# Kernel optimization log

Measured on AMD Instinct MI355X. Metric: run time of the kernel, lower is better.

Reference implementation:

```python
import jax, jax.numpy as jnp
import numpy as np

EPS = 1e-6


def setup_inputs() -> dict:
    key = jax.random.key(0)
    ks = jax.random.split(key, 10)
    N1, N2, K, E, LAYERS = 4096, 4096, 10, 262144, 3
    D = 2 ** K  # 1024
    us = jax.random.uniform(ks[0], (LAYERS, N1, D), dtype=jnp.float32)
    vs = jax.random.uniform(ks[1], (LAYERS, N2, D), dtype=jnp.float32)
    gamma = jax.random.normal(ks[2], (N1, LAYERS), dtype=jnp.float32)
    delta = jax.random.normal(ks[3], (N2, LAYERS), dtype=jnp.float32)
    latent_z1 = jax.random.uniform(ks[4], (N1, LAYERS), dtype=jnp.float32)
    latent_w1 = jax.random.uniform(ks[5], (N2, LAYERS), dtype=jnp.float32)
    # p_k_l initialized as log(uniform) in torch; any real values are valid params
    p_ks = jnp.full((LAYERS, K + 1), jnp.log(1.0 / (K + 1)), dtype=jnp.float32)
    p_ks = p_ks + 0.01 * jax.random.normal(ks[6], (LAYERS, K + 1), dtype=jnp.float32)
    L_ = 5.0 * jnp.ones((1,), dtype=jnp.float32)
    sparse_is = jax.random.randint(ks[7], (LAYERS, E), 0, N1, dtype=jnp.int64) if jax.config.jax_enable_x64 else jax.random.randint(ks[7], (LAYERS, E), 0, N1).astype(jnp.int32)
    sparse_js = jax.random.randint(ks[8], (LAYERS, E), 0, N2).astype(sparse_is.dtype)
    return {"us": us, "vs": vs, "gamma": gamma, "delta": delta,
            "latent_z1": latent_z1, "latent_w1": latent_w1,
            "p_ks": p_ks, "L_": L_,
            "sparse_is": sparse_is, "sparse_js": sparse_js}


def reference(us, vs, gamma, delta, latent_z1, latent_w1, p_ks, L_, sparse_is, sparse_js):
    LAYERS, N1, D = us.shape
    N2 = vs.shape[1]
    K = p_ks.shape[1] - 1  # tree_height
    latent_z = jax.nn.softmax(latent_z1, axis=1)  # Softmax(dim=1)
    latent_w = jax.nn.softmax(latent_w1, axis=1)
    L = jax.nn.softplus(L_)[0]
    ll = jnp.float32(0.0)
    for layer in range(LAYERS):
        p_k = jax.nn.softmax(p_ks[layer], axis=0)  # soft_0
        g = gamma[:, layer]                         # [N1]
        d = delta[:, layer]                         # [N2]
        emb_z = jax.nn.softmax(us[layer], axis=1)   # [N1, D]
        emb_w = jax.nn.softmax(vs[layer], axis=1)   # [N2, D]
        # hierarchical tree-weighted similarity: sum of GEMMs at coarsening levels
        inter = p_k[0] * jnp.ones((N1, N2), dtype=us.dtype)
        z_k, w_k = emb_z, emb_w
        for k in range(1, K):
            z_k = z_k.reshape(N1, -1, 2).sum(axis=2)  # [N1, D/2^k]
            w_k = w_k.reshape(N2, -1, 2).sum(axis=2)  # [N2, D/2^k]
            inter = inter + p_k[k] * jnp.einsum('nd,md->nm', z_k, w_k + EPS)
        inter = inter + p_k[K] * jnp.einsum('nd,md->nm', emb_z, emb_w + EPS)
        mat_1 = g[:, None] + d[None, :]                              # [N1, N2]
        mat_0 = (latent_z[:, layer][:, None] * L) * (latent_w[:, layer] + EPS)[None, :] * inter
        mat = jax.nn.softplus(mat_0 + mat_1)
        z_pdist1 = mat.sum()
        if N1 == N2:  # remove diagonal contributions
            z_pdist1 = z_pdist1 - jnp.trace(mat)
        i_ = sparse_is[layer]
        j_ = sparse_js[layer]
        z_pdist2 = (mat_0[i_, j_] + mat_1[i_, j_]).sum()
        ll = ll + (z_pdist2 - z_pdist1)
    return ll
```

## Files before the change

### kernel.cpp

```cpp
#include <hip/hip_runtime.h>
#include <hip/hip_bf16.h>
#include <stdint.h>

#define EPSV 1e-6f
#define N1 4096
#define N2 4096
#define DD 1024
#define NLAYERS 3
#define KKC 10

typedef __bf16 bf16_t;
typedef __bf16 bf16x8 __attribute__((ext_vector_type(8)));
typedef float f32x4 __attribute__((ext_vector_type(4)));
typedef long longx2 __attribute__((ext_vector_type(2)));

#define ZSCALE 256.0f
#define WSCALE 64.0f
#define INVSCALE 6.103515625e-05f

#define NBIN_L 1024
#define NBIN_T (NLAYERS*NBIN_L)

__device__ __forceinline__ float softplus_fast(float x) {
  return fmaxf(x, 0.f) + __logf(1.f + __expf(-fabsf(x)));
}
__device__ __forceinline__ float softplus_ref(float x) {
  return fmaxf(x, 0.f) + log1pf(expf(-fabsf(x)));
}
__device__ __forceinline__ float wredsum(float x) {
  #pragma unroll
  for (int o = 32; o; o >>= 1) x += __shfl_xor(x, o, 64);
  return x;
}
__device__ __forceinline__ float wredmax(float x) {
  #pragma unroll
  for (int o = 32; o; o >>= 1) x = fmaxf(x, __shfl_xor(x, o, 64));
  return x;
}
__device__ __forceinline__ void global_load_lds16(const void* g, void* l) {
  __builtin_amdgcn_global_load_lds(
      (const __attribute__((address_space(1))) uint32_t*)g,
      (__attribute__((address_space(3))) uint32_t*)l, 16, 0, 0);
}

__device__ __forceinline__ uint32_t enc_e4m3(float x) {
  if (x < 0.015625f) return (uint32_t)__float2int_rn(x * 512.0f);
  uint32_t u = __float_as_uint(x);
  u += 0x7FFFFu + ((u >> 20) & 1u);
  return (((u >> 23) - 120u) << 3) | ((u >> 20) & 7u);
}

__global__ __launch_bounds__(256) void prep_small(
    const float* __restrict__ lz, const float* __restrict__ lw,
    const float* __restrict__ gamma, const float* __restrict__ delta,
    const float* __restrict__ pks, const float* __restrict__ Lp,
    float* __restrict__ consts, float* __restrict__ a_tab, float* __restrict__ b_tab,
    float* __restrict__ g_tab, float* __restrict__ d_tab,
    uint32_t* __restrict__ hist, float* __restrict__ out)
{
  int n = blockIdx.x * blockDim.x + threadIdx.x;
  float Lv = softplus_ref(Lp[0]);
  if (n == 0) out[0] = 0.f;
  if (n < NBIN_T) hist[n] = 0u;
  if (n < N1) {
    float z0 = lz[n*3], z1 = lz[n*3+1], z2 = lz[n*3+2];
    float m = fmaxf(z0, fmaxf(z1, z2));
    float e0 = expf(z0-m), e1 = expf(z1-m), e2 = expf(z2-m);
    float inv = 1.f/(e0+e1+e2);
    a_tab[0*N1+n] = e0*inv*Lv; a_tab[1*N1+n] = e1*inv*Lv; a_tab[2*N1+n] = e2*inv*Lv;
    float w0 = lw[n*3], w1 = lw[n*3+1], w2 = lw[n*3+2];
    m = fmaxf(w0, fmaxf(w1, w2));
    e0 = expf(w0-m); e1 = expf(w1-m); e2 = expf(w2-m);
    inv = 1.f/(e0+e1+e2);
    b_tab[0*N2+n] = e0*inv+EPSV; b_tab[1*N2+n] = e1*inv+EPSV; b_tab[2*N2+n] = e2*inv+EPSV;
    #pragma unroll
    for (int k = 0; k < 3; ++k) {
      g_tab[k*N1+n] = gamma[n*3+k];
      d_tab[k*N2+n] = delta[n*3+k];
    }
  }
  if (n < NLAYERS) {
    float p[KKC+1]; float m = -1e30f;
    for (int k = 0; k <= KKC; ++k) { p[k] = pks[n*(KKC+1)+k]; m = fmaxf(m, p[k]); }
    float s = 0.f;
    for (int k = 0; k <= KKC; ++k) { p[k] = expf(p[k]-m); s += p[k]; }
    float inv = 1.f/s;
    for (int k = 0; k <= KKC; ++k) consts[8 + n*(KKC+1) + k] = p[k]*inv;
    consts[n] = p[0]*inv + EPSV*(1.f - p[0]*inv);
  }
}

#define EPB 2048

__global__ __launch_bounds__(256) void edge_hist(
    const int* __restrict__ is_, const int* __restrict__ js_,
    uint32_t* __restrict__ hist, int E)
{
  __shared__ uint32_t h[NBIN_L];
  const int lay = blockIdx.y;
  const int t = threadIdx.x;
  #pragma unroll
  for (int i = 0; i < NBIN_L/256; ++i) h[t + i*256] = 0u;
  __syncthreads();
  const int e0 = blockIdx.x * EPB;
  const int e1 = min(e0 + EPB, E);
  for (int e = e0 + t; e < e1; e += 256) {
    int i = is_[(size_t)lay*E + e], j = js_[(size_t)lay*E + e];
    atomicAdd(&h[(i>>7)*32 + (j>>7)], 1u);
  }
  __syncthreads();
  #pragma unroll
  for (int i = 0; i < NBIN_L/256; ++i)
    if (h[t + i*256]) atomicAdd(&hist[lay*NBIN_L + t + i*256], h[t + i*256]);
}

__global__ __launch_bounds__(256) void edge_scan(
    const uint32_t* __restrict__ hist, uint32_t* __restrict__ off,
    uint32_t* __restrict__ cursor)
{
  __shared__ uint32_t sa[NBIN_T], sb[NBIN_T];
  const int t = threadIdx.x;
  for (int i = t; i < NBIN_T; i += 256) sa[i] = hist[i];
  __syncthreads();
  uint32_t* src = sa; uint32_t* dst = sb;
  for (int s = 1; s < NBIN_T; s <<= 1) {
    for (int i = t; i < NBIN_T; i += 256) dst[i] = src[i] + (i >= s ? src[i-s] : 0u);
    __syncthreads();
    uint32_t* tmp = src; src = dst; dst = tmp;
  }
  for (int i = t; i < NBIN_T; i += 256) {
    uint32_t ex = i ? src[i-1] : 0u;
    off[i] = ex; cursor[i] = ex;
  }
  if (t == 0) off[NBIN_T] = src[NBIN_T-1];
}

__global__ __launch_bounds__(256) void edge_scatter(
    const int* __restrict__ is_, const int* __restrict__ js_,
    uint32_t* __restrict__ cursor, uint16_t* __restrict__ ebuf, int E)
{
  __shared__ uint32_t h[NBIN_L];
  __shared__ uint32_t basev[NBIN_L];
  const int lay = blockIdx.y;
  const int t = threadIdx.x;
  #pragma unroll
  for (int i = 0; i < NBIN_L/256; ++i) h[t + i*256] = 0u;
  __syncthreads();
  const int e0 = blockIdx.x * EPB;
  const int e1 = min(e0 + EPB, E);
  for (int e = e0 + t; e < e1; e += 256) {
    int i = is_[(size_t)lay*E + e], j = js_[(size_t)lay*E + e];
    atomicAdd(&h[(i>>7)*32 + (j>>7)], 1u);
  }
  __syncthreads();
  #pragma unroll
  for (int i = 0; i < NBIN_L/256; ++i) {
    int b = t + i*256;
    basev[b] = h[b] ? atomicAdd(&cursor[lay*NBIN_L + b], h[b]) : 0u;
    h[b] = 0u;
  }
  __syncthreads();
  for (int e = e0 + t; e < e1; e += 256) {
    int i = is_[(size_t)lay*E + e], j = js_[(size_t)lay*E + e];
    int b = (i>>7)*32 + (j>>7);
    uint32_t r = atomicAdd(&h[b], 1u);
    ebuf[basev[b] + r] = (uint16_t)(((i & 127) << 7) | (j & 127));
  }
}

__global__ __launch_bounds__(256) void prep_rows(
    const float* __restrict__ us, const float* __restrict__ vs,
    uint8_t* __restrict__ zt8, uint8_t* __restrict__ wt8, size_t lstride,
    const float* __restrict__ consts, int layer0)
{
  const int t = threadIdx.x, w = t >> 6, l = t & 63;
  const int n = blockIdx.x*4 + w;
  const int layer = layer0 + blockIdx.y;
  const int zmode = (blockIdx.z == 0);
  const float* src = (zmode ? us : vs) + ((size_t)layer*N1 + n)*DD + l*16;
  uint8_t* drow = (zmode ? zt8 : wt8) + (size_t)blockIdx.y*lstride + (size_t)n*1024;
  const int p0 = (l>>2)*64 + ((l&1)*2)*16 + ((l&3)>>1)*8;

  float e[16];
  {
    const float4* s4 = (const float4*)src;
    float4 u0 = s4[0], u1 = s4[1], u2 = s4[2], u3 = s4[3];
    e[0]=u0.x; e[1]=u0.y; e[2]=u0.z; e[3]=u0.w;
    e[4]=u1.x; e[5]=u1.y; e[6]=u1.z; e[7]=u1.w;
    e[8]=u2.x; e[9]=u2.y; e[10]=u2.z; e[11]=u2.w;
    e[12]=u3.x; e[13]=u3.y; e[14]=u3.z; e[15]=u3.w;
  }
  float mx = e[0];
  #pragma unroll
  for (int i = 1; i < 16; ++i) mx = fmaxf(mx, e[i]);
  mx = wredmax(mx);
  float s = 0.f;
  #pragma unroll
  for (int i = 0; i < 16; ++i) { e[i] = __expf(e[i]-mx); s += e[i]; }
  s = wredsum(s);
  float inv = 1.f/s;
  #pragma unroll
  for (int i = 0; i < 16; ++i) e[i] *= inv;

  uint32_t b4[4] = {0u, 0u, 0u, 0u};
  if (!zmode) {
    #pragma unroll
    for (int i = 0; i < 16; ++i)
      b4[i>>2] |= enc_e4m3(e[i]*WSCALE) << ((i&3)*8);
  } else {
    float s1[8], s2[4], s3[2], s4v;
    #pragma unroll
    for (int i = 0; i < 8; ++i) s1[i] = e[2*i] + e[2*i+1];
    #pragma unroll
    for (int i = 0; i < 4; ++i) s2[i] = s1[2*i] + s1[2*i+1];
    s3[0] = s2[0]+s2[1]; s3[1] = s2[2]+s2[3];
    s4v = s3[0]+s3[1];
    float s5 = s4v + __shfl_xor(s4v, 1, 64);
    float s6 = s5  + __shfl_xor(s5, 2, 64);
    float s7 = s6  + __shfl_xor(s6, 4, 64);
    float s8 = s7  + __shfl_xor(s7, 8, 64);
    float s9 = s8  + __shfl_xor(s8, 16, 64);
    const float* pk = consts + 8 + layer*(KKC+1);
    const float base = pk[4]*s4v + pk[5]*s5 + pk[6]*s6 + pk[7]*s7 + pk[8]*s8 + pk[9]*s9;
    const float p1 = pk[1], p2 = pk[2], p3 = pk[3], p10 = pk[10];
    #pragma unroll
    for (int i = 0; i < 16; ++i) {
      float v = p10*e[i] + p1*s1[i>>1] + p2*s2[i>>2] + p3*s3[i>>3] + base;
      b4[i>>2] |= enc_e4m3(v*ZSCALE) << ((i&3)*8);
    }
  }
  uint64_t u0 = (uint64_t)b4[0] | ((uint64_t)b4[1] << 32);
  uint64_t u1 = (uint64_t)b4[2] | ((uint64_t)b4[3] << 32);
  *(uint64_t*)(drow + p0)      = u0;
  *(uint64_t*)(drow + p0 + 16) = u1;
}

__global__ __launch_bounds__(256, 4) void gemm_fused(
    const uint8_t* __restrict__ Az8, size_t zls,
    const uint8_t* __restrict__ Bw8, size_t wls,
    const float* __restrict__ a_tab, const float* __restrict__ b_tab,
    const float* __restrict__ g_tab, const float* __restrict__ d_tab,
    const float* __restrict__ consts, int layer0,
    const uint32_t* __restrict__ eoff, const uint16_t* __restrict__ ebuf,
    float* __restrict__ out)
{
  extern __shared__ char lds[];
  const int t = threadIdx.x;
  const int w = t >> 6, l = t & 63;
  const int wm = w >> 1, wn = w & 1;
  const int fr = l & 15, fq = l >> 4;

  const int nbx = gridDim.x, nby = gridDim.y;
  int lid = blockIdx.x + nbx*(blockIdx.y + nby*blockIdx.z);
  const int nblk = nbx*nby*gridDim.z;
  const int cpx = nblk >> 3;
  int nid = (lid & 7)*cpx + (lid >> 3);
  const int bz = nid / (nbx*nby);
  const int rem = nid % (nbx*nby);
  const int bi = rem % nbx, bj = rem / nbx;

  const int i0 = bi*128, j0 = bj*128;
  const int layer = layer0 + bz;
  Az8 += (size_t)bz*zls + (size_t)i0*1024;
  Bw8 += (size_t)bz*wls + (size_t)j0*1024;

  f32x4 acc[4][4];
  f32x4 zero = {0.f, 0.f, 0.f, 0.f};
  #pragma unroll
  for (int m = 0; m < 4; ++m)
    #pragma unroll
    for (int nn = 0; nn < 4; ++nn) acc[m][nn] = zero;

  const int go = (l & 7) ^ (l >> 3);
  const size_t s_off = (size_t)((l >> 3)*2 + (go >> 2))*1024 + (size_t)(go & 3)*16;
  const int slot = (((fr & 1) << 2) + fq) ^ (fr >> 1);
  const int abase = wm*4096 + (fr>>1)*128 + slot*16;
  const int bbase = 8192 + wn*4096 + (fr>>1)*128 + slot*16;

  longx2 ar2[4], br2[4];

#define STG_A(tile) do { \
    char* _d = lds + ((tile)&1)*16384 + w*2048; \
    const uint8_t* _s = Az8 + (size_t)(w*32)*1024 + (size_t)(tile)*64 + s_off; \
    global_load_lds16(_s, _d); \
    global_load_lds16(_s + (size_t)16*1024, _d + 1024); \
  } while (0)
#define STG_B(tile) do { \
    char* _d = lds + ((tile)&1)*16384 + 8192 + w*2048; \
    const uint8_t* _s = Bw8 + (size_t)(w*32)*1024 + (size_t)(tile)*64 + s_off; \
    global_load_lds16(_s, _d); \
    global_load_lds16(_s + (size_t)16*1024, _d + 1024); \
  } while (0)

  STG_A(0); STG_B(0);

  for (int u = 0; u < 16; ++u) {
    const int cb = (u & 1)*16384;
    asm volatile("s_waitcnt vmcnt(0)" ::: "memory");
    asm volatile("s_barrier" ::: "memory");
    #pragma unroll
    for (int i = 0; i < 4; ++i)
      ar2[i] = *(const longx2*)(lds + cb + abase + i*1024);
    #pragma unroll
    for (int j = 0; j < 4; ++j)
      br2[j] = *(const longx2*)(lds + cb + bbase + j*1024);
    if (u < 15) { STG_A(u+1); STG_B(u+1); }
    __builtin_amdgcn_s_setprio(1);
    #pragma unroll
    for (int i = 0; i < 4; ++i)
      #pragma unroll
      for (int j = 0; j < 4; ++j) {
        acc[i][j] = __builtin_amdgcn_mfma_f32_16x16x32_fp8_fp8(
            ar2[i].x, br2[j].x, acc[i][j], 0, 0, 0);
        acc[i][j] = __builtin_amdgcn_mfma_f32_16x16x32_fp8_fp8(
            ar2[i].y, br2[j].y, acc[i][j], 0, 0, 0);
      }
    __builtin_amdgcn_s_setprio(0);
  }
#undef STG_A
#undef STG_B

  __syncthreads();
  const float cc = consts[layer];
  {
    char* cbase = lds + wm*16384 + fq*1024 + wn*128 + fr*2;
    #pragma unroll
    for (int m = 0; m < 4; ++m)
      #pragma unroll
      for (int nn = 0; nn < 4; ++nn)
        #pragma unroll
        for (int r = 0; r < 4; ++r)
          *(bf16_t*)(cbase + m*4096 + r*256 + nn*32) =
              (bf16_t)(acc[m][nn][r]*INVSCALE + cc);
  }
  __syncthreads();

  const float* at = a_tab + layer*N1;
  const float* bt = b_tab + layer*N2;
  const float* gt = g_tab + layer*N1;
  const float* dt = d_tab + layer*N2;
  float dsum = 0.f;
  #pragma unroll
  for (int i = 0; i < 8; ++i) {
    const int id = t + i*256;
    const int row = id >> 4, g = id & 15;
    bf16x8 v = *(const bf16x8*)(lds + row*256 + g*16);
    const int grow = i0 + row, gcol = j0 + g*8;
    const float av = at[grow], gv = gt[grow];
    float4 b0 = *(const float4*)(bt + gcol), b1 = *(const float4*)(bt + gcol + 4);
    float4 d0 = *(const float4*)(dt + gcol), d1 = *(const float4*)(dt + gcol + 4);
    float bb[8] = {b0.x,b0.y,b0.z,b0.w,b1.x,b1.y,b1.z,b1.w};
    float dd[8] = {d0.x,d0.y,d0.z,d0.w,d1.x,d1.y,d1.z,d1.w};
    #pragma unroll
    for (int e2 = 0; e2 < 8; ++e2) {
      float x = av*bb[e2]*(float)v[e2] + gv + dd[e2];
      float sp = softplus_fast(x);
      dsum += (grow != gcol + e2) ? sp : 0.f;
    }
  }
  const int bin = bz*NBIN_L + bi*32 + bj;
  const uint32_t e0 = eoff[bin], e1 = eoff[bin+1];
  float ssum = 0.f;
  for (uint32_t e = e0 + (uint32_t)t; e < e1; e += 256u) {
    const int pk2 = ebuf[e];
    const int li = pk2 >> 7, lj = pk2 & 127;
    float dc = (float)*(const bf16_t*)(lds + li*256 + lj*2);
    ssum += at[i0+li]*bt[j0+lj]*dc + gt[i0+li] + dt[j0+lj];
  }
  float tot = wredsum(ssum - dsum);
  __syncthreads();
  if (l == 0) ((float*)lds)[w] = tot;
  __syncthreads();
  if (t == 0) {
    const float* r = (const float*)lds;
    atomicAdd(out, r[0] + r[1] + r[2] + r[3]);
  }
}

extern "C" void kernel_launch(void* const* d_in, const int* in_sizes, int n_in,
                              void* d_out, int out_size, void* d_ws, size_t ws_size,
                              hipStream_t stream) {
  const float* us    = (const float*)d_in[0];
  const float* vs    = (const float*)d_in[1];
  const float* gamma = (const float*)d_in[2];
  const float* delta = (const float*)d_in[3];
  const float* lz    = (const float*)d_in[4];
  const float* lw    = (const float*)d_in[5];
  const float* pks   = (const float*)d_in[6];
  const float* Lp    = (const float*)d_in[7];
  const int*   sis   = (const int*)d_in[8];
  const int*   sjs   = (const int*)d_in[9];
  float* out = (float*)d_out;
  char*  ws  = (char*)d_ws;
  const int E = in_sizes[8] / NLAYERS;

  size_t p = 0;
  float* consts = (float*)(ws + p); p += 1024;
  float* a_tab  = (float*)(ws + p); p += (size_t)NLAYERS*N1*4;
  float* b_tab  = (float*)(ws + p); p += (size_t)NLAYERS*N2*4;
  float* g_tab  = (float*)(ws + p); p += (size_t)NLAYERS*N1*4;
  float* d_tab  = (float*)(ws + p); p += (size_t)NLAYERS*N2*4;
  uint32_t* hist   = (uint32_t*)(ws + p); p += 4096*4;
  uint32_t* eoff   = (uint32_t*)(ws + p); p += 4096*4;
  uint32_t* cursor = (uint32_t*)(ws + p); p += 4096*4;
  uint16_t* ebuf   = (uint16_t*)(ws + p); p += (size_t)NLAYERS*E*2;
  p = (p + 4095) & ~(size_t)4095;
  uint8_t* zt8 = (uint8_t*)(ws + p); p += (size_t)NLAYERS*N1*1024;
  uint8_t* wt8 = (uint8_t*)(ws + p); p += (size_t)NLAYERS*N2*1024;
  if (ws_size < p) return;
  const size_t ZLS = (size_t)N1*1024;
  const size_t LDSB = 32768;
  const int nebl = (E + EPB - 1) / EPB;

  prep_small<<<(N1+255)/256, 256, 0, stream>>>(lz, lw, gamma, delta, pks, Lp,
                                               consts, a_tab, b_tab, g_tab, d_tab,
                                               hist, out);
  edge_hist<<<dim3(nebl, NLAYERS), 256, 0, stream>>>(sis, sjs, hist, E);
  edge_scan<<<1, 256, 0, stream>>>(hist, eoff, cursor);
  edge_scatter<<<dim3(nebl, NLAYERS), 256, 0, stream>>>(sis, sjs, cursor, ebuf, E);
  prep_rows<<<dim3(N1/4, NLAYERS, 2), 256, 0, stream>>>(us, vs, zt8, wt8, ZLS, consts, 0);
  gemm_fused<<<dim3(32,32,NLAYERS), 256, LDSB, stream>>>(
      zt8, ZLS, wt8, ZLS, a_tab, b_tab, g_tab, d_tab, consts, 0, eoff, ebuf, out);
}
```

Measured before the change: 140.8 us.

## Triple-buffer GEMM LDS staging and parallelize edge scan per layer

The fused FP8 GEMM main loop moves from double to triple buffering. It prefetches two K-tiles ahead and waits with vmcnt(4) instead of draining all loads, so global-to-LDS transfers overlap more with MFMA work. Dynamic LDS grows from 32 KB to 48 KB per block, which may reduce occupancy. The edge prefix scan now runs one block per layer over 1024 bins and adds a per-layer base offset of lay*E, which shortens a serial single-block kernel.

```diff
diff --git a/kernel.cpp b/kernel.cpp
--- a/kernel.cpp
+++ b/kernel.cpp
@@ -116,23 +116,25 @@
 
 __global__ __launch_bounds__(256) void edge_scan(
     const uint32_t* __restrict__ hist, uint32_t* __restrict__ off,
-    uint32_t* __restrict__ cursor)
-{
-  __shared__ uint32_t sa[NBIN_T], sb[NBIN_T];
+    uint32_t* __restrict__ cursor, int E)
+{
+  __shared__ uint32_t sa[NBIN_L], sb[NBIN_L];
+  const int lay = blockIdx.x;
   const int t = threadIdx.x;
-  for (int i = t; i < NBIN_T; i += 256) sa[i] = hist[i];
+  const uint32_t base = (uint32_t)lay * (uint32_t)E;
+  for (int i = t; i < NBIN_L; i += 256) sa[i] = hist[lay*NBIN_L + i];
   __syncthreads();
   uint32_t* src = sa; uint32_t* dst = sb;
-  for (int s = 1; s < NBIN_T; s <<= 1) {
-    for (int i = t; i < NBIN_T; i += 256) dst[i] = src[i] + (i >= s ? src[i-s] : 0u);
+  for (int s = 1; s < NBIN_L; s <<= 1) {
+    for (int i = t; i < NBIN_L; i += 256) dst[i] = src[i] + (i >= s ? src[i-s] : 0u);
     __syncthreads();
     uint32_t* tmp = src; src = dst; dst = tmp;
   }
-  for (int i = t; i < NBIN_T; i += 256) {
-    uint32_t ex = i ? src[i-1] : 0u;
-    off[i] = ex; cursor[i] = ex;
-  }
-  if (t == 0) off[NBIN_T] = src[NBIN_T-1];
+  for (int i = t; i < NBIN_L; i += 256) {
+    uint32_t ex = base + (i ? src[i-1] : 0u);
+    off[lay*NBIN_L + i] = ex; cursor[lay*NBIN_L + i] = ex;
+  }
+  if (t == 0 && lay == NLAYERS-1) off[NBIN_T] = base + src[NBIN_L-1];
 }
 
 __global__ __launch_bounds__(256) void edge_scatter(
@@ -279,24 +281,27 @@
 
   longx2 ar2[4], br2[4];
 
-#define STG_A(tile) do { \
-    char* _d = lds + ((tile)&1)*16384 + w*2048; \
+#define STG_A(tile, buf) do { \
+    char* _d = lds + (buf)*16384 + w*2048; \
     const uint8_t* _s = Az8 + (size_t)(w*32)*1024 + (size_t)(tile)*64 + s_off; \
     global_load_lds16(_s, _d); \
     global_load_lds16(_s + (size_t)16*1024, _d + 1024); \
   } while (0)
-#define STG_B(tile) do { \
-    char* _d = lds + ((tile)&1)*16384 + 8192 + w*2048; \
+#define STG_B(tile, buf) do { \
+    char* _d = lds + (buf)*16384 + 8192 + w*2048; \
     const uint8_t* _s = Bw8 + (size_t)(w*32)*1024 + (size_t)(tile)*64 + s_off; \
     global_load_lds16(_s, _d); \
     global_load_lds16(_s + (size_t)16*1024, _d + 1024); \
   } while (0)
 
-  STG_A(0); STG_B(0);
-
+  STG_A(0, 0); STG_B(0, 0);
+  STG_A(1, 1); STG_B(1, 1);
+
+  #pragma unroll
   for (int u = 0; u < 16; ++u) {
-    const int cb = (u & 1)*16384;
-    asm volatile("s_waitcnt vmcnt(0)" ::: "memory");
+    const int cb = (u % 3)*16384;
+    if (u < 15) asm volatile("s_waitcnt vmcnt(4)" ::: "memory");
+    else        asm volatile("s_waitcnt vmcnt(0)" ::: "memory");
     asm volatile("s_barrier" ::: "memory");
     #pragma unroll
     for (int i = 0; i < 4; ++i)
@@ -304,7 +309,7 @@
     #pragma unroll
     for (int j = 0; j < 4; ++j)
       br2[j] = *(const longx2*)(lds + cb + bbase + j*1024);
-    if (u < 15) { STG_A(u+1); STG_B(u+1); }
+    if (u <= 13) { STG_A(u+2, (u+2)%3); STG_B(u+2, (u+2)%3); }
     __builtin_amdgcn_s_setprio(1);
     #pragma unroll
     for (int i = 0; i < 4; ++i)
@@ -409,14 +414,14 @@
   uint8_t* wt8 = (uint8_t*)(ws + p); p += (size_t)NLAYERS*N2*1024;
   if (ws_size < p) return;
   const size_t ZLS = (size_t)N1*1024;
-  const size_t LDSB = 32768;
+  const size_t LDSB = 49152;
   const int nebl = (E + EPB - 1) / EPB;
 
   prep_small<<<(N1+255)/256, 256, 0, stream>>>(lz, lw, gamma, delta, pks, Lp,
                                                consts, a_tab, b_tab, g_tab, d_tab,
                                                hist, out);
   edge_hist<<<dim3(nebl, NLAYERS), 256, 0, stream>>>(sis, sjs, hist, E);
-  edge_scan<<<1, 256, 0, stream>>>(hist, eoff, cursor);
+  edge_scan<<<NLAYERS, 256, 0, stream>>>(hist, eoff, cursor, E);
   edge_scatter<<<dim3(nebl, NLAYERS), 256, 0, stream>>>(sis, sjs, cursor, ebuf, E);
   prep_rows<<<dim3(N1/4, NLAYERS, 2), 256, 0, stream>>>(us, vs, zt8, wt8, ZLS, consts, 0);
   gemm_fused<<<dim3(32,32,NLAYERS), 256, LDSB, stream>>>(
```

Result: faster. 135.3 us (-3.9%).
